# Performance work log

Measured on AMD Instinct MI355X. Metric: run time of the kernel, lower is better.

## Reference

```python
import jax, jax.numpy as jnp
import numpy as np

T, D = 8192, 256   # frames, feature dim
P, K = 64, 128     # phone vocabulary, centers per phone


def setup_inputs() -> dict:
    key = jax.random.key(0)
    k1, k2, k3 = jax.random.split(key, 3)
    h = jax.random.normal(k1, (T, D), dtype=jnp.float32)
    centers = jax.random.normal(k2, (P, K, D), dtype=jnp.float32)
    phones = jax.random.randint(k3, (T,), 0, P, dtype=jnp.int64)
    return {"h": h, "centers": centers, "phones": phones}


def reference(h, centers, phones):
    """Per-phone 1-NN retrieval: for each frame t, find nearest center in the
    pool for phones[t] and return that center (anonymized feature).
    centers: [P, K, D] padded table replacing the (pattern, phone, gender) dict.
    """
    c = centers[phones]                                # [T, K, D] irregular gather
    # squared euclidean distance; ||h_t||^2 is constant per row -> omit for argmin
    d2 = jnp.sum(c * c, axis=-1) - 2.0 * jnp.einsum("td,tkd->tk", h, c)  # [T, K]
    idx = jnp.argmin(d2, axis=-1)                      # [T]
    h_anon = jnp.take_along_axis(c, idx[:, None, None], axis=1)[:, 0, :]  # [T, D]
    return h_anon
```

## Files before the change

### kernel.cpp

```cpp
#include <hip/hip_runtime.h>

#define T_FRAMES 8192
#define D_DIM    256
#define P_PHONES 64
#define K_CENT   128
#define TILE_F   16
#define BUCKET_CAP 256
#define SLOTS_PP   16
#define MARGIN   1.0f
#define NC_MAX   4

#define WS_NORMS  0
#define WS_FIDX   32768
#define WS_SCNT   98304
#define WS_HH     102400
#define WS_CH     (102400 + 4194304)

typedef _Float16 half8 __attribute__((ext_vector_type(8)));
typedef float    f32x4 __attribute__((ext_vector_type(4)));

__global__ __launch_bounds__(1024) void qr_prep_kernel(const float* __restrict__ h,
                                                       const float* __restrict__ centers,
                                                       const int* __restrict__ phones,
                                                       float* __restrict__ norms,
                                                       int* __restrict__ fidx,
                                                       int* __restrict__ slotcnt,
                                                       _Float16* __restrict__ hH,
                                                       _Float16* __restrict__ cH) {
    const int b    = blockIdx.x;
    const int tid  = threadIdx.x;
    const int w    = tid >> 6;
    const int lane = tid & 63;

    if (b < 512) {
        const size_t e = ((size_t)b * 1024 + tid) * 4;
        union { _Float16 hf[4]; uint2 u; } pk;
        float4 v = *(const float4*)(h + e);
        pk.hf[0] = (_Float16)(-2.f * v.x); pk.hf[1] = (_Float16)(-2.f * v.y);
        pk.hf[2] = (_Float16)(-2.f * v.z); pk.hf[3] = (_Float16)(-2.f * v.w);
        *(uint2*)(hH + e) = pk.u;
        v = *(const float4*)(centers + e);
        pk.hf[0] = (_Float16)v.x; pk.hf[1] = (_Float16)v.y;
        pk.hf[2] = (_Float16)v.z; pk.hf[3] = (_Float16)v.w;
        *(uint2*)(cH + e) = pk.u;
        float s = v.x * v.x + v.y * v.y + v.z * v.z + v.w * v.w;
#pragma unroll
        for (int off = 32; off; off >>= 1) s += __shfl_xor(s, off, 64);
        if (lane == 0) norms[b * 16 + w] = s;
        return;
    }

    __shared__ int nsh;
    __shared__ int sF0;
    const int j = b - 512;
    if (tid == 0) { nsh = 0; sF0 = 0; }
    __syncthreads();
#pragma unroll
    for (int ch = 0; ch < 8; ++ch) {
        const int f = w * 512 + ch * 64 + lane;
        const bool mt = (phones[f] == j);
        const unsigned long long mask = __ballot(mt);
        const int cnt = __popcll(mask);
        if (cnt) {
            int base = 0;
            if (lane == 0) base = atomicAdd(&nsh, cnt);
            base = __shfl(base, 0, 64);
            if (mt) {
                const int pos = base + __popcll(mask & ((1ull << lane) - 1ull));
                if (pos < BUCKET_CAP) fidx[j * BUCKET_CAP + pos] = f;
                if (pos == 0) sF0 = f;
            }
        }
    }
    __syncthreads();
    const int c = nsh > BUCKET_CAP ? BUCKET_CAP : nsh;
    const int f0 = sF0;
    for (int pos = c + tid; pos < BUCKET_CAP; pos += 1024) fidx[j * BUCKET_CAP + pos] = f0;
    if (tid < SLOTS_PP) {
        const int rem = c - tid * TILE_F;
        slotcnt[j * SLOTS_PP + tid] = rem < 0 ? 0 : (rem > TILE_F ? TILE_F : rem);
    }
}

__global__ __launch_bounds__(256, 4) void qr_main_kernel(const float* __restrict__ h,
                                                         const float* __restrict__ centers,
                                                         const float* __restrict__ norms,
                                                         const int* __restrict__ fidx,
                                                         const int* __restrict__ slotcnt,
                                                         const _Float16* __restrict__ hH,
                                                         const _Float16* __restrict__ cH,
                                                         float* __restrict__ out) {
    __shared__ float sMin[4][TILE_F];
    __shared__ int   sNc[TILE_F];
    __shared__ int   sCl[TILE_F][NC_MAX];
    __shared__ int   sWin[TILE_F];
    __shared__ int   sRl[TILE_F];
    __shared__ int   sRn;

    const int bid  = blockIdx.x;
    const int slot = ((bid & 7) << 7) | (bid >> 3);
    const int p    = slot >> 4;

    const int tid  = threadIdx.x;
    const int wave = tid >> 6;
    const int lane = tid & 63;
    const int m    = lane & 15;
    const int quad = lane >> 4;

    if (tid == 0) sRn = 0;
    if (tid < TILE_F) sNc[tid] = 0;

    const int fcnt = slotcnt[slot];
    const int fiA  = fidx[slot * TILE_F + m];
    if (fcnt == 0) return;

    half8 aF[8];
    const _Float16* ap = hH + ((size_t)fiA << 8) + quad * 8;
#pragma unroll
    for (int s = 0; s < 8; ++s) aF[s] = *(const half8*)(ap + s * 32);

    half8 bF[2][8];
    const _Float16* bp = cH + (((size_t)(p << 7) + (wave << 5) + m) << 8) + quad * 8;
#pragma unroll
    for (int ch = 0; ch < 2; ++ch)
#pragma unroll
        for (int s = 0; s < 8; ++s)
            bF[ch][s] = *(const half8*)(bp + (ch << 12) + s * 32);

    const float nrm0 = norms[(p << 7) + (wave << 5) + m];
    const float nrm1 = norms[(p << 7) + (wave << 5) + 16 + m];
    __builtin_amdgcn_sched_barrier(0);

    f32x4 acc[2];
    acc[0] = f32x4{nrm0, nrm0, nrm0, nrm0};
    acc[1] = f32x4{nrm1, nrm1, nrm1, nrm1};
#pragma unroll
    for (int s = 0; s < 8; ++s) {
        acc[0] = __builtin_amdgcn_mfma_f32_16x16x32_f16(aF[s], bF[0][s], acc[0], 0, 0, 0);
        acc[1] = __builtin_amdgcn_mfma_f32_16x16x32_f16(aF[s], bF[1][s], acc[1], 0, 0, 0);
    }

#pragma unroll
    for (int r = 0; r < 4; ++r) {
        float mn = fminf(acc[0][r], acc[1][r]);
#pragma unroll
        for (int off = 1; off <= 8; off <<= 1) mn = fminf(mn, __shfl_xor(mn, off, 64));
        if (m == 0) sMin[wave][quad * 4 + r] = mn;
    }
    __syncthreads();

#pragma unroll
    for (int r = 0; r < 4; ++r) {
        const int f = quad * 4 + r;
        const float gm = fminf(fminf(sMin[0][f], sMin[1][f]), fminf(sMin[2][f], sMin[3][f]));
        const float tau = gm + MARGIN;
#pragma unroll
        for (int ch = 0; ch < 2; ++ch) {
            if (acc[ch][r] < tau) {
                const int pos = atomicAdd(&sNc[f], 1);
                if (pos < NC_MAX) sCl[f][pos] = (wave << 5) + ch * 16 + m;
            }
        }
    }
    __syncthreads();

    if (tid < TILE_F) {
        if (sNc[tid] == 1) sWin[tid] = sCl[tid][0];
        else if (tid < fcnt) sRl[atomicAdd(&sRn, 1)] = tid;
    }
    __syncthreads();

    const int rn = sRn;
    for (int ridx = wave; ridx < rn; ridx += 4) {
        const int f2 = sRl[ridx];
        const int fi = fidx[slot * TILE_F + f2];
        const int tc = sNc[f2];
        if (tc <= NC_MAX) {
            int cl[NC_MAX];
            cl[0] = sCl[f2][0];
#pragma unroll
            for (int k = 1; k < NC_MAX; ++k) cl[k] = (k < tc) ? sCl[f2][k] : cl[0];
            const float4 hv = ((const float4*)(h + (size_t)fi * D_DIM))[lane];
            float4 cv[NC_MAX];
#pragma unroll
            for (int k = 0; k < NC_MAX; ++k)
                cv[k] = ((const float4*)(centers + ((size_t)(p << 7) + cl[k]) * D_DIM))[lane];
            float s[NC_MAX];
#pragma unroll
            for (int k = 0; k < NC_MAX; ++k)
                s[k] = hv.x * cv[k].x + hv.y * cv[k].y + hv.z * cv[k].z + hv.w * cv[k].w;
#pragma unroll
            for (int off = 1; off < 64; off <<= 1)
#pragma unroll
                for (int k = 0; k < NC_MAX; ++k) s[k] += __shfl_xor(s[k], off, 64);
            float best = norms[(p << 7) + cl[0]] - 2.f * s[0];
            int   bc   = cl[0];
#pragma unroll
            for (int k = 1; k < NC_MAX; ++k) {
                const float dk = norms[(p << 7) + cl[k]] - 2.f * s[k];
                if (dk < best || (dk == best && cl[k] < bc)) { best = dk; bc = cl[k]; }
            }
            if (lane == 0) sWin[f2] = bc;
        } else {
            const float4* hp  = (const float4*)(h + (size_t)fi * D_DIM);
            const float4* cp0 = (const float4*)(centers + ((size_t)(p << 7) + lane) * D_DIM);
            float s0 = 0.f, s1 = 0.f;
#pragma unroll 4
            for (int jx = 0; jx < 64; ++jx) {
                const float4 a  = hp[jx];
                const float4 b0 = cp0[jx];
                const float4 b1 = cp0[jx + 4096];
                s0 += a.x * b0.x + a.y * b0.y + a.z * b0.z + a.w * b0.w;
                s1 += a.x * b1.x + a.y * b1.y + a.z * b1.z + a.w * b1.w;
            }
            float best = norms[(p << 7) + lane] - 2.f * s0;
            int   bc   = lane;
            const float d1 = norms[(p << 7) + lane + 64] - 2.f * s1;
            if (d1 < best) { best = d1; bc = lane + 64; }
#pragma unroll
            for (int off = 1; off < 64; off <<= 1) {
                const float ob = __shfl_xor(best, off, 64);
                const int   oc = __shfl_xor(bc, off, 64);
                if (ob < best || (ob == best && oc < bc)) { best = ob; bc = oc; }
            }
            if (lane == 0) sWin[f2] = bc;
        }
    }
    __syncthreads();

    const int f = tid >> 4, part = tid & 15;
    if (f < fcnt) {
        const int fo = fidx[slot * TILE_F + f];
        const float4* src = (const float4*)(centers + ((size_t)(p << 7) + sWin[f]) * D_DIM);
        float4*       dst = (float4*)(out + (size_t)fo * D_DIM);
#pragma unroll
        for (int jx = 0; jx < 4; ++jx) dst[part + 16 * jx] = src[part + 16 * jx];
    }
}

extern "C" void kernel_launch(void* const* d_in, const int* in_sizes, int n_in,
                              void* d_out, int out_size, void* d_ws, size_t ws_size,
                              hipStream_t stream) {
    const float* h       = (const float*)d_in[0];
    const float* centers = (const float*)d_in[1];
    const int*   phones  = (const int*)d_in[2];
    float*       out     = (float*)d_out;

    char* ws = (char*)d_ws;
    float*    norms   = (float*)(ws + WS_NORMS);
    int*      fidx    = (int*)(ws + WS_FIDX);
    int*      slotcnt = (int*)(ws + WS_SCNT);
    _Float16* hH      = (_Float16*)(ws + WS_HH);
    _Float16* cH      = (_Float16*)(ws + WS_CH);

    qr_prep_kernel<<<576, 1024, 0, stream>>>(h, centers, phones, norms, fidx, slotcnt, hH, cH);
    qr_main_kernel<<<P_PHONES * SLOTS_PP, 256, 0, stream>>>(h, centers, norms, fidx, slotcnt, hH, cH, out);
}
```

Baseline: 90.83 us.

## Fuse prep into main kernel with in-block phone bucketing and on-the-fly fp16 conversion

Removes the separate prep kernel. Each block now scans all phones itself to find its 16 frames via a prefix scan, converts h and centers to fp16 in registers, and computes center norms locally into shared memory. This drops one kernel launch and the workspace round trip for the fp16 copies, norms and bucket indices. In exchange every block redundantly reads the full 8192-entry phones array and recomputes norms for its phone's 128 centers, which 16 blocks per phone repeat.

```diff
diff --git a/kernel.cpp b/kernel.cpp
--- a/kernel.cpp
+++ b/kernel.cpp
@@ -5,91 +5,20 @@
 #define P_PHONES 64
 #define K_CENT   128
 #define TILE_F   16
-#define BUCKET_CAP 256
-#define SLOTS_PP   16
+#define SLOTS_PP 16
 #define MARGIN   1.0f
 #define NC_MAX   4
 
-#define WS_NORMS  0
-#define WS_FIDX   32768
-#define WS_SCNT   98304
-#define WS_HH     102400
-#define WS_CH     (102400 + 4194304)
-
 typedef _Float16 half8 __attribute__((ext_vector_type(8)));
 typedef float    f32x4 __attribute__((ext_vector_type(4)));
 
-__global__ __launch_bounds__(1024) void qr_prep_kernel(const float* __restrict__ h,
-                                                       const float* __restrict__ centers,
-                                                       const int* __restrict__ phones,
-                                                       float* __restrict__ norms,
-                                                       int* __restrict__ fidx,
-                                                       int* __restrict__ slotcnt,
-                                                       _Float16* __restrict__ hH,
-                                                       _Float16* __restrict__ cH) {
-    const int b    = blockIdx.x;
-    const int tid  = threadIdx.x;
-    const int w    = tid >> 6;
-    const int lane = tid & 63;
-
-    if (b < 512) {
-        const size_t e = ((size_t)b * 1024 + tid) * 4;
-        union { _Float16 hf[4]; uint2 u; } pk;
-        float4 v = *(const float4*)(h + e);
-        pk.hf[0] = (_Float16)(-2.f * v.x); pk.hf[1] = (_Float16)(-2.f * v.y);
-        pk.hf[2] = (_Float16)(-2.f * v.z); pk.hf[3] = (_Float16)(-2.f * v.w);
-        *(uint2*)(hH + e) = pk.u;
-        v = *(const float4*)(centers + e);
-        pk.hf[0] = (_Float16)v.x; pk.hf[1] = (_Float16)v.y;
-        pk.hf[2] = (_Float16)v.z; pk.hf[3] = (_Float16)v.w;
-        *(uint2*)(cH + e) = pk.u;
-        float s = v.x * v.x + v.y * v.y + v.z * v.z + v.w * v.w;
-#pragma unroll
-        for (int off = 32; off; off >>= 1) s += __shfl_xor(s, off, 64);
-        if (lane == 0) norms[b * 16 + w] = s;
-        return;
-    }
-
-    __shared__ int nsh;
-    __shared__ int sF0;
-    const int j = b - 512;
-    if (tid == 0) { nsh = 0; sF0 = 0; }
-    __syncthreads();
-#pragma unroll
-    for (int ch = 0; ch < 8; ++ch) {
-        const int f = w * 512 + ch * 64 + lane;
-        const bool mt = (phones[f] == j);
-        const unsigned long long mask = __ballot(mt);
-        const int cnt = __popcll(mask);
-        if (cnt) {
-            int base = 0;
-            if (lane == 0) base = atomicAdd(&nsh, cnt);
-            base = __shfl(base, 0, 64);
-            if (mt) {
-                const int pos = base + __popcll(mask & ((1ull << lane) - 1ull));
-                if (pos < BUCKET_CAP) fidx[j * BUCKET_CAP + pos] = f;
-                if (pos == 0) sF0 = f;
-            }
-        }
-    }
-    __syncthreads();
-    const int c = nsh > BUCKET_CAP ? BUCKET_CAP : nsh;
-    const int f0 = sF0;
-    for (int pos = c + tid; pos < BUCKET_CAP; pos += 1024) fidx[j * BUCKET_CAP + pos] = f0;
-    if (tid < SLOTS_PP) {
-        const int rem = c - tid * TILE_F;
-        slotcnt[j * SLOTS_PP + tid] = rem < 0 ? 0 : (rem > TILE_F ? TILE_F : rem);
-    }
-}
-
-__global__ __launch_bounds__(256, 4) void qr_main_kernel(const float* __restrict__ h,
-                                                         const float* __restrict__ centers,
-                                                         const float* __restrict__ norms,
-                                                         const int* __restrict__ fidx,
-                                                         const int* __restrict__ slotcnt,
-                                                         const _Float16* __restrict__ hH,
-                                                         const _Float16* __restrict__ cH,
-                                                         float* __restrict__ out) {
+__global__ __launch_bounds__(256, 4) void qr_fused_kernel(const float* __restrict__ h,
+                                                          const float* __restrict__ centers,
+                                                          const int* __restrict__ phones,
+                                                          float* __restrict__ out) {
+    __shared__ int   sWT[4];
+    __shared__ int   sFid[TILE_F];
+    __shared__ float sNorm[K_CENT];
     __shared__ float sMin[4][TILE_F];
     __shared__ int   sNc[TILE_F];
     __shared__ int   sCl[TILE_F][NC_MAX];
@@ -100,6 +29,7 @@
     const int bid  = blockIdx.x;
     const int slot = ((bid & 7) << 7) | (bid >> 3);
     const int p    = slot >> 4;
+    const int wlo  = (slot & 15) << 4;
 
     const int tid  = threadIdx.x;
     const int wave = tid >> 6;
@@ -110,25 +40,84 @@
     if (tid == 0) sRn = 0;
     if (tid < TILE_F) sNc[tid] = 0;
 
-    const int fcnt = slotcnt[slot];
-    const int fiA  = fidx[slot * TILE_F + m];
+    const int fbase = wave * 2048 + lane * 32;
+    int4 pq[8];
+#pragma unroll
+    for (int q = 0; q < 8; ++q) pq[q] = ((const int4*)(phones + fbase))[q];
+    int cl = 0;
+#pragma unroll
+    for (int q = 0; q < 8; ++q)
+        cl += (pq[q].x == p) + (pq[q].y == p) + (pq[q].z == p) + (pq[q].w == p);
+    int scan = cl;
+#pragma unroll
+    for (int off = 1; off < 64; off <<= 1) {
+        const int t = __shfl_up(scan, off, 64);
+        if (lane >= off) scan += t;
+    }
+    if (lane == 63) sWT[wave] = scan;
+    __syncthreads();
+    int bb = 0, T = 0;
+#pragma unroll
+    for (int w2 = 0; w2 < 4; ++w2) { const int v = sWT[w2]; T += v; if (w2 < wave) bb += v; }
+    {
+        int run = bb + (scan - cl);
+        const int whi = wlo + TILE_F;
+#define QR_STEP(VV, FOFF) { if ((VV) == p) { if (run >= wlo && run < whi) sFid[run - wlo] = fbase + (FOFF); ++run; } }
+#pragma unroll
+        for (int q = 0; q < 8; ++q) {
+            QR_STEP(pq[q].x, q * 4 + 0)
+            QR_STEP(pq[q].y, q * 4 + 1)
+            QR_STEP(pq[q].z, q * 4 + 2)
+            QR_STEP(pq[q].w, q * 4 + 3)
+        }
+#undef QR_STEP
+    }
+    __syncthreads();
+    const int fcnt = min(max(T - wlo, 0), TILE_F);
     if (fcnt == 0) return;
 
+    const int fiA = sFid[min(m, fcnt - 1)];
+
     half8 aF[8];
-    const _Float16* ap = hH + ((size_t)fiA << 8) + quad * 8;
-#pragma unroll
-    for (int s = 0; s < 8; ++s) aF[s] = *(const half8*)(ap + s * 32);
+    {
+        const float* ap = h + (size_t)fiA * D_DIM + quad * 8;
+#pragma unroll
+        for (int s = 0; s < 8; ++s) {
+            const float4 l4 = *(const float4*)(ap + s * 32);
+            const float4 h4 = *(const float4*)(ap + s * 32 + 4);
+            half8 t;
+            t[0] = (_Float16)(-2.f * l4.x); t[1] = (_Float16)(-2.f * l4.y);
+            t[2] = (_Float16)(-2.f * l4.z); t[3] = (_Float16)(-2.f * l4.w);
+            t[4] = (_Float16)(-2.f * h4.x); t[5] = (_Float16)(-2.f * h4.y);
+            t[6] = (_Float16)(-2.f * h4.z); t[7] = (_Float16)(-2.f * h4.w);
+            aF[s] = t;
+        }
+    }
 
     half8 bF[2][8];
-    const _Float16* bp = cH + (((size_t)(p << 7) + (wave << 5) + m) << 8) + quad * 8;
-#pragma unroll
-    for (int ch = 0; ch < 2; ++ch)
-#pragma unroll
-        for (int s = 0; s < 8; ++s)
-            bF[ch][s] = *(const half8*)(bp + (ch << 12) + s * 32);
-
-    const float nrm0 = norms[(p << 7) + (wave << 5) + m];
-    const float nrm1 = norms[(p << 7) + (wave << 5) + 16 + m];
+    float nrm0 = 0.f, nrm1 = 0.f;
+#pragma unroll
+    for (int ch = 0; ch < 2; ++ch) {
+        const float* bp = centers + ((size_t)((p << 7) + (wave << 5) + ch * 16 + m)) * D_DIM + quad * 8;
+        float accn = 0.f;
+#pragma unroll
+        for (int s = 0; s < 8; ++s) {
+            const float4 l4 = *(const float4*)(bp + s * 32);
+            const float4 h4 = *(const float4*)(bp + s * 32 + 4);
+            half8 t;
+            t[0] = (_Float16)l4.x; t[1] = (_Float16)l4.y;
+            t[2] = (_Float16)l4.z; t[3] = (_Float16)l4.w;
+            t[4] = (_Float16)h4.x; t[5] = (_Float16)h4.y;
+            t[6] = (_Float16)h4.z; t[7] = (_Float16)h4.w;
+            bF[ch][s] = t;
+            accn += l4.x * l4.x + l4.y * l4.y + l4.z * l4.z + l4.w * l4.w
+                  + h4.x * h4.x + h4.y * h4.y + h4.z * h4.z + h4.w * h4.w;
+        }
+        accn += __shfl_xor(accn, 16, 64);
+        accn += __shfl_xor(accn, 32, 64);
+        if (ch == 0) nrm0 = accn; else nrm1 = accn;
+        if (quad == 0) sNorm[(wave << 5) + ch * 16 + m] = accn;
+    }
     __builtin_amdgcn_sched_barrier(0);
 
     f32x4 acc[2];
@@ -173,18 +162,18 @@
     const int rn = sRn;
     for (int ridx = wave; ridx < rn; ridx += 4) {
         const int f2 = sRl[ridx];
-        const int fi = fidx[slot * TILE_F + f2];
+        const int fi = sFid[f2];
         const int tc = sNc[f2];
         if (tc <= NC_MAX) {
-            int cl[NC_MAX];
-            cl[0] = sCl[f2][0];
-#pragma unroll
-            for (int k = 1; k < NC_MAX; ++k) cl[k] = (k < tc) ? sCl[f2][k] : cl[0];
+            int cnd[NC_MAX];
+            cnd[0] = sCl[f2][0];
+#pragma unroll
+            for (int k = 1; k < NC_MAX; ++k) cnd[k] = (k < tc) ? sCl[f2][k] : cnd[0];
             const float4 hv = ((const float4*)(h + (size_t)fi * D_DIM))[lane];
             float4 cv[NC_MAX];
 #pragma unroll
             for (int k = 0; k < NC_MAX; ++k)
-                cv[k] = ((const float4*)(centers + ((size_t)(p << 7) + cl[k]) * D_DIM))[lane];
+                cv[k] = ((const float4*)(centers + ((size_t)(p << 7) + cnd[k]) * D_DIM))[lane];
             float s[NC_MAX];
 #pragma unroll
             for (int k = 0; k < NC_MAX; ++k)
@@ -193,12 +182,12 @@
             for (int off = 1; off < 64; off <<= 1)
 #pragma unroll
                 for (int k = 0; k < NC_MAX; ++k) s[k] += __shfl_xor(s[k], off, 64);
-            float best = norms[(p << 7) + cl[0]] - 2.f * s[0];
-            int   bc   = cl[0];
+            float best = sNorm[cnd[0]] - 2.f * s[0];
+            int   bc   = cnd[0];
 #pragma unroll
             for (int k = 1; k < NC_MAX; ++k) {
-                const float dk = norms[(p << 7) + cl[k]] - 2.f * s[k];
-                if (dk < best || (dk == best && cl[k] < bc)) { best = dk; bc = cl[k]; }
+                const float dk = sNorm[cnd[k]] - 2.f * s[k];
+                if (dk < best || (dk == best && cnd[k] < bc)) { best = dk; bc = cnd[k]; }
             }
             if (lane == 0) sWin[f2] = bc;
         } else {
@@ -213,9 +202,9 @@
                 s0 += a.x * b0.x + a.y * b0.y + a.z * b0.z + a.w * b0.w;
                 s1 += a.x * b1.x + a.y * b1.y + a.z * b1.z + a.w * b1.w;
             }
-            float best = norms[(p << 7) + lane] - 2.f * s0;
+            float best = sNorm[lane] - 2.f * s0;
             int   bc   = lane;
-            const float d1 = norms[(p << 7) + lane + 64] - 2.f * s1;
+            const float d1 = sNorm[lane + 64] - 2.f * s1;
             if (d1 < best) { best = d1; bc = lane + 64; }
 #pragma unroll
             for (int off = 1; off < 64; off <<= 1) {
@@ -230,7 +219,7 @@
 
     const int f = tid >> 4, part = tid & 15;
     if (f < fcnt) {
-        const int fo = fidx[slot * TILE_F + f];
+        const int fo = sFid[f];
         const float4* src = (const float4*)(centers + ((size_t)(p << 7) + sWin[f]) * D_DIM);
         float4*       dst = (float4*)(out + (size_t)fo * D_DIM);
 #pragma unroll
@@ -245,14 +234,7 @@
     const float* centers = (const float*)d_in[1];
     const int*   phones  = (const int*)d_in[2];
     float*       out     = (float*)d_out;
-
-    char* ws = (char*)d_ws;
-    float*    norms   = (float*)(ws + WS_NORMS);
-    int*      fidx    = (int*)(ws + WS_FIDX);
-    int*      slotcnt = (int*)(ws + WS_SCNT);
-    _Float16* hH      = (_Float16*)(ws + WS_HH);
-    _Float16* cH      = (_Float16*)(ws + WS_CH);
-
-    qr_prep_kernel<<<576, 1024, 0, stream>>>(h, centers, phones, norms, fidx, slotcnt, hH, cH);
-    qr_main_kernel<<<P_PHONES * SLOTS_PP, 256, 0, stream>>>(h, centers, norms, fidx, slotcnt, hH, cH, out);
+    (void)d_ws; (void)ws_size;
+
+    qr_fused_kernel<<<P_PHONES * SLOTS_PP, 256, 0, stream>>>(h, centers, phones, out);
 }
```

Result: slower. 125.8 us (+38.5%).

## Convert frames to fp16 inside main kernel and process 32 frames per block

Applied to the files above, without the earlier changes.

The separate fp16 conversion of h in the prep kernel is removed; the main kernel now loads fp32 frame rows, scales them by -2 and converts them to half in registers. Each block now handles 32 frames, two 16-row A tiles, so every center fragment loaded from global memory is reused across two MFMA tiles. The prep kernel shrinks to 128 center-conversion blocks plus the bucketing blocks. This removes a full write and re-read of an fp16 copy of h and halves the number of main-kernel blocks, at the cost of more register pressure and fewer blocks to spread across the GPU.

```diff
diff --git a/kernel.cpp b/kernel.cpp
--- a/kernel.cpp
+++ b/kernel.cpp
@@ -4,55 +4,51 @@
 #define D_DIM    256
 #define P_PHONES 64
 #define K_CENT   128
-#define TILE_F   16
+#define TILE_F   32
 #define BUCKET_CAP 256
-#define SLOTS_PP   16
+#define SLOTS_PP   8
 #define MARGIN   1.0f
 #define NC_MAX   4
 
 #define WS_NORMS  0
 #define WS_FIDX   32768
 #define WS_SCNT   98304
-#define WS_HH     102400
-#define WS_CH     (102400 + 4194304)
+#define WS_CH     102400
 
 typedef _Float16 half8 __attribute__((ext_vector_type(8)));
 typedef float    f32x4 __attribute__((ext_vector_type(4)));
 
-__global__ __launch_bounds__(1024) void qr_prep_kernel(const float* __restrict__ h,
-                                                       const float* __restrict__ centers,
+__global__ __launch_bounds__(1024) void qr_prep_kernel(const float* __restrict__ centers,
                                                        const int* __restrict__ phones,
                                                        float* __restrict__ norms,
                                                        int* __restrict__ fidx,
                                                        int* __restrict__ slotcnt,
-                                                       _Float16* __restrict__ hH,
                                                        _Float16* __restrict__ cH) {
     const int b    = blockIdx.x;
     const int tid  = threadIdx.x;
     const int w    = tid >> 6;
     const int lane = tid & 63;
 
-    if (b < 512) {
-        const size_t e = ((size_t)b * 1024 + tid) * 4;
-        union { _Float16 hf[4]; uint2 u; } pk;
-        float4 v = *(const float4*)(h + e);
-        pk.hf[0] = (_Float16)(-2.f * v.x); pk.hf[1] = (_Float16)(-2.f * v.y);
-        pk.hf[2] = (_Float16)(-2.f * v.z); pk.hf[3] = (_Float16)(-2.f * v.w);
-        *(uint2*)(hH + e) = pk.u;
-        v = *(const float4*)(centers + e);
-        pk.hf[0] = (_Float16)v.x; pk.hf[1] = (_Float16)v.y;
-        pk.hf[2] = (_Float16)v.z; pk.hf[3] = (_Float16)v.w;
-        *(uint2*)(cH + e) = pk.u;
-        float s = v.x * v.x + v.y * v.y + v.z * v.z + v.w * v.w;
-#pragma unroll
-        for (int off = 32; off; off >>= 1) s += __shfl_xor(s, off, 64);
-        if (lane == 0) norms[b * 16 + w] = s;
+    if (b < 128) {
+#pragma unroll
+        for (int k = 0; k < 4; ++k) {
+            const size_t e = (size_t)b * 16384 + (size_t)k * 4096 + (size_t)tid * 4;
+            const float4 v = *(const float4*)(centers + e);
+            union { _Float16 hf[4]; uint2 u; } pk;
+            pk.hf[0] = (_Float16)v.x; pk.hf[1] = (_Float16)v.y;
+            pk.hf[2] = (_Float16)v.z; pk.hf[3] = (_Float16)v.w;
+            *(uint2*)(cH + e) = pk.u;
+            float s = v.x * v.x + v.y * v.y + v.z * v.z + v.w * v.w;
+#pragma unroll
+            for (int off = 32; off; off >>= 1) s += __shfl_xor(s, off, 64);
+            if (lane == 0) norms[b * 64 + k * 16 + w] = s;
+        }
         return;
     }
 
     __shared__ int nsh;
     __shared__ int sF0;
-    const int j = b - 512;
+    const int j = b - 128;
     if (tid == 0) { nsh = 0; sF0 = 0; }
     __syncthreads();
 #pragma unroll
@@ -87,7 +83,6 @@
                                                          const float* __restrict__ norms,
                                                          const int* __restrict__ fidx,
                                                          const int* __restrict__ slotcnt,
-                                                         const _Float16* __restrict__ hH,
                                                          const _Float16* __restrict__ cH,
                                                          float* __restrict__ out) {
     __shared__ float sMin[4][TILE_F];
@@ -98,8 +93,9 @@
     __shared__ int   sRn;
 
     const int bid  = blockIdx.x;
-    const int slot = ((bid & 7) << 7) | (bid >> 3);
-    const int p    = slot >> 4;
+    const int slot = ((bid & 7) << 6) | (bid >> 3);
+    const int p    = slot >> 3;
+    const int base = (p << 8) + (slot & 7) * TILE_F;
 
     const int tid  = threadIdx.x;
     const int wave = tid >> 6;
@@ -111,56 +107,103 @@
     if (tid < TILE_F) sNc[tid] = 0;
 
     const int fcnt = slotcnt[slot];
-    const int fiA  = fidx[slot * TILE_F + m];
+    const int fi0  = fidx[base + m];
+    const int fi1  = fidx[base + 16 + m];
     if (fcnt == 0) return;
 
-    half8 aF[8];
-    const _Float16* ap = hH + ((size_t)fiA << 8) + quad * 8;
-#pragma unroll
-    for (int s = 0; s < 8; ++s) aF[s] = *(const half8*)(ap + s * 32);
-
-    half8 bF[2][8];
-    const _Float16* bp = cH + (((size_t)(p << 7) + (wave << 5) + m) << 8) + quad * 8;
-#pragma unroll
-    for (int ch = 0; ch < 2; ++ch)
-#pragma unroll
-        for (int s = 0; s < 8; ++s)
-            bF[ch][s] = *(const half8*)(bp + (ch << 12) + s * 32);
-
-    const float nrm0 = norms[(p << 7) + (wave << 5) + m];
-    const float nrm1 = norms[(p << 7) + (wave << 5) + 16 + m];
+    half8 aF0[8], aF1[8];
+    {
+        const float* ap = h + (size_t)fi0 * D_DIM + quad * 8;
+#pragma unroll
+        for (int s = 0; s < 8; ++s) {
+            const float4 l4 = *(const float4*)(ap + s * 32);
+            const float4 h4 = *(const float4*)(ap + s * 32 + 4);
+            half8 t;
+            t[0] = (_Float16)(-2.f * l4.x); t[1] = (_Float16)(-2.f * l4.y);
+            t[2] = (_Float16)(-2.f * l4.z); t[3] = (_Float16)(-2.f * l4.w);
+            t[4] = (_Float16)(-2.f * h4.x); t[5] = (_Float16)(-2.f * h4.y);
+            t[6] = (_Float16)(-2.f * h4.z); t[7] = (_Float16)(-2.f * h4.w);
+            aF0[s] = t;
+        }
+    }
     __builtin_amdgcn_sched_barrier(0);
-
-    f32x4 acc[2];
-    acc[0] = f32x4{nrm0, nrm0, nrm0, nrm0};
-    acc[1] = f32x4{nrm1, nrm1, nrm1, nrm1};
-#pragma unroll
-    for (int s = 0; s < 8; ++s) {
-        acc[0] = __builtin_amdgcn_mfma_f32_16x16x32_f16(aF[s], bF[0][s], acc[0], 0, 0, 0);
-        acc[1] = __builtin_amdgcn_mfma_f32_16x16x32_f16(aF[s], bF[1][s], acc[1], 0, 0, 0);
+    {
+        const float* ap = h + (size_t)fi1 * D_DIM + quad * 8;
+#pragma unroll
+        for (int s = 0; s < 8; ++s) {
+            const float4 l4 = *(const float4*)(ap + s * 32);
+            const float4 h4 = *(const float4*)(ap + s * 32 + 4);
+            half8 t;
+            t[0] = (_Float16)(-2.f * l4.x); t[1] = (_Float16)(-2.f * l4.y);
+            t[2] = (_Float16)(-2.f * l4.z); t[3] = (_Float16)(-2.f * l4.w);
+            t[4] = (_Float16)(-2.f * h4.x); t[5] = (_Float16)(-2.f * h4.y);
+            t[6] = (_Float16)(-2.f * h4.z); t[7] = (_Float16)(-2.f * h4.w);
+            aF1[s] = t;
+        }
+    }
+    __builtin_amdgcn_sched_barrier(0);
+
+    f32x4 acc00, acc01, acc10, acc11;
+    {
+        const _Float16* bp = cH + (((size_t)(p << 7) + (wave << 5) + m) << 8) + quad * 8;
+        half8 bF[8];
+#pragma unroll
+        for (int s = 0; s < 8; ++s) bF[s] = *(const half8*)(bp + s * 32);
+        const float nrm = norms[(p << 7) + (wave << 5) + m];
+        __builtin_amdgcn_sched_barrier(0);
+        acc00 = f32x4{nrm, nrm, nrm, nrm};
+        acc10 = f32x4{nrm, nrm, nrm, nrm};
+#pragma unroll
+        for (int s = 0; s < 8; ++s) {
+            acc00 = __builtin_amdgcn_mfma_f32_16x16x32_f16(aF0[s], bF[s], acc00, 0, 0, 0);
+            acc10 = __builtin_amdgcn_mfma_f32_16x16x32_f16(aF1[s], bF[s], acc10, 0, 0, 0);
+        }
+    }
+    __builtin_amdgcn_sched_barrier(0);
+    {
+        const _Float16* bp = cH + (((size_t)(p << 7) + (wave << 5) + 16 + m) << 8) + quad * 8;
+        half8 bF[8];
+#pragma unroll
+        for (int s = 0; s < 8; ++s) bF[s] = *(const half8*)(bp + s * 32);
+        const float nrm = norms[(p << 7) + (wave << 5) + 16 + m];
+        __builtin_amdgcn_sched_barrier(0);
+        acc01 = f32x4{nrm, nrm, nrm, nrm};
+        acc11 = f32x4{nrm, nrm, nrm, nrm};
+#pragma unroll
+        for (int s = 0; s < 8; ++s) {
+            acc01 = __builtin_amdgcn_mfma_f32_16x16x32_f16(aF0[s], bF[s], acc01, 0, 0, 0);
+            acc11 = __builtin_amdgcn_mfma_f32_16x16x32_f16(aF1[s], bF[s], acc11, 0, 0, 0);
+        }
     }
 
 #pragma unroll
     for (int r = 0; r < 4; ++r) {
-        float mn = fminf(acc[0][r], acc[1][r]);
-#pragma unroll
-        for (int off = 1; off <= 8; off <<= 1) mn = fminf(mn, __shfl_xor(mn, off, 64));
-        if (m == 0) sMin[wave][quad * 4 + r] = mn;
+        float mn0 = fminf(acc00[r], acc01[r]);
+        float mn1 = fminf(acc10[r], acc11[r]);
+#pragma unroll
+        for (int off = 1; off <= 8; off <<= 1) {
+            mn0 = fminf(mn0, __shfl_xor(mn0, off, 64));
+            mn1 = fminf(mn1, __shfl_xor(mn1, off, 64));
+        }
+        if (m == 0) {
+            sMin[wave][quad * 4 + r]      = mn0;
+            sMin[wave][16 + quad * 4 + r] = mn1;
+        }
     }
     __syncthreads();
 
 #pragma unroll
     for (int r = 0; r < 4; ++r) {
-        const int f = quad * 4 + r;
-        const float gm = fminf(fminf(sMin[0][f], sMin[1][f]), fminf(sMin[2][f], sMin[3][f]));
-        const float tau = gm + MARGIN;
-#pragma unroll
-        for (int ch = 0; ch < 2; ++ch) {
-            if (acc[ch][r] < tau) {
-                const int pos = atomicAdd(&sNc[f], 1);
-                if (pos < NC_MAX) sCl[f][pos] = (wave << 5) + ch * 16 + m;
-            }
-        }
+        const int f0f = quad * 4 + r;
+        const int f1f = 16 + quad * 4 + r;
+        const float gm0 = fminf(fminf(sMin[0][f0f], sMin[1][f0f]), fminf(sMin[2][f0f], sMin[3][f0f]));
+        const float gm1 = fminf(fminf(sMin[0][f1f], sMin[1][f1f]), fminf(sMin[2][f1f], sMin[3][f1f]));
+        const float tau0 = gm0 + MARGIN;
+        const float tau1 = gm1 + MARGIN;
+        if (acc00[r] < tau0) { const int pos = atomicAdd(&sNc[f0f], 1); if (pos < NC_MAX) sCl[f0f][pos] = (wave << 5) + m; }
+        if (acc01[r] < tau0) { const int pos = atomicAdd(&sNc[f0f], 1); if (pos < NC_MAX) sCl[f0f][pos] = (wave << 5) + 16 + m; }
+        if (acc10[r] < tau1) { const int pos = atomicAdd(&sNc[f1f], 1); if (pos < NC_MAX) sCl[f1f][pos] = (wave << 5) + m; }
+        if (acc11[r] < tau1) { const int pos = atomicAdd(&sNc[f1f], 1); if (pos < NC_MAX) sCl[f1f][pos] = (wave << 5) + 16 + m; }
     }
     __syncthreads();
 
@@ -173,18 +216,18 @@
     const int rn = sRn;
     for (int ridx = wave; ridx < rn; ridx += 4) {
         const int f2 = sRl[ridx];
-        const int fi = fidx[slot * TILE_F + f2];
+        const int fi = fidx[base + f2];
         const int tc = sNc[f2];
         if (tc <= NC_MAX) {
-            int cl[NC_MAX];
-            cl[0] = sCl[f2][0];
-#pragma unroll
-            for (int k = 1; k < NC_MAX; ++k) cl[k] = (k < tc) ? sCl[f2][k] : cl[0];
+            int cnd[NC_MAX];
+            cnd[0] = sCl[f2][0];
+#pragma unroll
+            for (int k = 1; k < NC_MAX; ++k) cnd[k] = (k < tc) ? sCl[f2][k] : cnd[0];
             const float4 hv = ((const float4*)(h + (size_t)fi * D_DIM))[lane];
             float4 cv[NC_MAX];
 #pragma unroll
             for (int k = 0; k < NC_MAX; ++k)
-                cv[k] = ((const float4*)(centers + ((size_t)(p << 7) + cl[k]) * D_DIM))[lane];
+                cv[k] = ((const float4*)(centers + ((size_t)(p << 7) + cnd[k]) * D_DIM))[lane];
             float s[NC_MAX];
 #pragma unroll
             for (int k = 0; k < NC_MAX; ++k)
@@ -193,12 +236,12 @@
             for (int off = 1; off < 64; off <<= 1)
 #pragma unroll
                 for (int k = 0; k < NC_MAX; ++k) s[k] += __shfl_xor(s[k], off, 64);
-            float best = norms[(p << 7) + cl[0]] - 2.f * s[0];
-            int   bc   = cl[0];
+            float best = norms[(p << 7) + cnd[0]] - 2.f * s[0];
+            int   bc   = cnd[0];
 #pragma unroll
             for (int k = 1; k < NC_MAX; ++k) {
-                const float dk = norms[(p << 7) + cl[k]] - 2.f * s[k];
-                if (dk < best || (dk == best && cl[k] < bc)) { best = dk; bc = cl[k]; }
+                const float dk = norms[(p << 7) + cnd[k]] - 2.f * s[k];
+                if (dk < best || (dk == best && cnd[k] < bc)) { best = dk; bc = cnd[k]; }
             }
             if (lane == 0) sWin[f2] = bc;
         } else {
@@ -228,13 +271,13 @@
     }
     __syncthreads();
 
-    const int f = tid >> 4, part = tid & 15;
+    const int f = tid >> 3, part = tid & 7;
     if (f < fcnt) {
-        const int fo = fidx[slot * TILE_F + f];
+        const int fo = fidx[base + f];
         const float4* src = (const float4*)(centers + ((size_t)(p << 7) + sWin[f]) * D_DIM);
         float4*       dst = (float4*)(out + (size_t)fo * D_DIM);
 #pragma unroll
-        for (int jx = 0; jx < 4; ++jx) dst[part + 16 * jx] = src[part + 16 * jx];
+        for (int jx = 0; jx < 8; ++jx) dst[part + 8 * jx] = src[part + 8 * jx];
     }
 }
 
@@ -250,9 +293,8 @@
     float*    norms   = (float*)(ws + WS_NORMS);
     int*      fidx    = (int*)(ws + WS_FIDX);
     int*      slotcnt = (int*)(ws + WS_SCNT);
-    _Float16* hH      = (_Float16*)(ws + WS_HH);
     _Float16* cH      = (_Float16*)(ws + WS_CH);
 
-    qr_prep_kernel<<<576, 1024, 0, stream>>>(h, centers, phones, norms, fidx, slotcnt, hH, cH);
-    qr_main_kernel<<<P_PHONES * SLOTS_PP, 256, 0, stream>>>(h, centers, norms, fidx, slotcnt, hH, cH, out);
+    qr_prep_kernel<<<192, 1024, 0, stream>>>(centers, phones, norms, fidx, slotcnt, cH);
+    qr_main_kernel<<<P_PHONES * SLOTS_PP, 256, 0, stream>>>(h, centers, norms, fidx, slotcnt, cH, out);
 }
```

Measured after the change: 94.95 us. +4.5%, slower.
